# Optimization experiments

Hardware: AMD Instinct MI355X
Metric: run time of the kernel (lower is better)

## Reference

```python
import jax, jax.numpy as jnp
import numpy as np

T = 32          # timesteps
GAIN = 1.0      # input_gain
TAU = 2.0       # LIF membrane time constant
VTH = 1.0       # v_threshold
VRESET = 0.0    # v_reset (hard reset)
ALPHA = 2.0     # ATan surrogate alpha


@jax.custom_vjp
def heaviside_atan(x):
    # forward: Heaviside spike; backward: ATan surrogate gradient
    return (x >= 0).astype(x.dtype)

def _hs_fwd(x):
    return heaviside_atan(x), x

def _hs_bwd(x, g):
    # d/dx ATan surrogate: (alpha/2) / (1 + (pi/2 * alpha * x)^2)
    return (g * (ALPHA / 2.0) / (1.0 + (jnp.pi / 2.0 * ALPHA * x) ** 2),)

heaviside_atan.defvjp(_hs_fwd, _hs_bwd)


def lif_multistep(cur_seq):
    """Multi-step LIF over cur_seq [T, B, H]; hard reset, detach_reset=True."""
    def step(v, x):
        # charge: v = v + (x - (v - v_reset)) / tau
        v = v + (x - (v - VRESET)) / TAU
        spike = heaviside_atan(v - VTH)
        sd = jax.lax.stop_gradient(spike)  # detach_reset
        v = (1.0 - sd) * v + sd * VRESET   # hard reset
        return v, spike

    v0 = jnp.full(cur_seq.shape[1:], VRESET, dtype=cur_seq.dtype)
    _, spikes = jax.lax.scan(step, v0, cur_seq)
    return spikes


def setup_inputs() -> dict:
    key = jax.random.key(0)
    ks = jax.random.split(key, 4)

    def xavier(k, o, i):
        lim = np.sqrt(6.0 / (i + o)).astype(np.float32)
        return jax.random.uniform(k, (o, i), minval=-lim, maxval=lim, dtype=jnp.float32)

    x_flat = jax.random.uniform(ks[0], (512, 784), dtype=jnp.float32)
    W0 = xavier(ks[1], 1024, 784)
    b0 = jnp.zeros((1024,), jnp.float32)
    W1 = xavier(ks[2], 1024, 1024)
    b1 = jnp.zeros((1024,), jnp.float32)
    W2 = xavier(ks[3], 10, 1024)
    b2 = jnp.zeros((10,), jnp.float32)
    return {"x_flat": x_flat, "W0": W0, "b0": b0, "W1": W1, "b1": b1, "W2": W2, "b2": b2}


def reference(x_flat, W0, b0, W1, b1, W2, b2):
    # repeat_static_input: [B, 784] -> [T, B, 784]
    h = jnp.broadcast_to(x_flat * GAIN, (T,) + x_flat.shape)
    count = None
    for W, b in ((W0, b0), (W1, b1), (W2, b2)):
        cur = jnp.einsum('tbi,oi->tbo', h, W) + b  # fc over all timesteps
        spk = lif_multistep(cur)                   # [T, B, out]
        count = spk.sum(axis=0)                    # spike counts [B, out]
        h = spk
    # predict() returns argmax(count); return the final count (logits) here
    return count
```

## Files before the change

kernel.cpp:

```cpp
#include <hip/hip_runtime.h>
#include <hip/hip_bf16.h>
#include <stdint.h>


typedef __bf16 bf16x8 __attribute__((ext_vector_type(8)));
typedef float  f32x4  __attribute__((ext_vector_type(4)));
typedef unsigned short u16x8 __attribute__((ext_vector_type(8)));

__device__ __forceinline__ unsigned short csel(float v, int sel) {
  __hip_bfloat16 h = __float2bfloat16(v);
  if (sel == 0) return __builtin_bit_cast(unsigned short, h);
  float r1 = v - __bfloat162float(h);
  __hip_bfloat16 m = __float2bfloat16(r1);
  if (sel == 1) return __builtin_bit_cast(unsigned short, m);
  float r2 = r1 - __bfloat162float(m);
  __hip_bfloat16 l = __float2bfloat16(r2);
  return __builtin_bit_cast(unsigned short, l);
}

__global__ __launch_bounds__(256, 2) void gemm0t_k(const float* __restrict__ x,
                                                   const float* __restrict__ W0,
                                                   const float* __restrict__ W1,
                                                   float* __restrict__ W1T,
                                                   float* __restrict__ Cpart) {
  __shared__ __align__(16) char smem[16512];
  const int bid = blockIdx.x, tid = threadIdx.x;

  if (bid >= 320) {
    float (*t)[33] = (float(*)[33])smem;
    int tt = bid - 320;
    int c0 = (tt & 31) * 32, r0 = (tt >> 5) * 32;
    int lx = tid & 31, ly = tid >> 5;
#pragma unroll
    for (int i = 0; i < 32; i += 8)
      t[ly + i][lx] = W1[(size_t)(r0 + ly + i) * 1024 + (c0 + lx)];
    __syncthreads();
#pragma unroll
    for (int i = 0; i < 32; i += 8)
      W1T[(size_t)(c0 + ly + i) * 1024 + (r0 + lx)] = t[lx][ly + i];
    return;
  }

  const int bx = bid & 3, by = (bid >> 2) & 7, bz = bid >> 5;
  const int wave = tid >> 6, lane = tid & 63, quad = lane >> 4, l16 = lane & 15;
  const int wm = (wave >> 1) * 64, wn = (wave & 1) * 64;
  const int mbase = bx * 128, nbase = by * 128, kbase = bz * 480;
  const int swz = (l16 >> 1) & 3;

  const int r = tid >> 1, h = tid & 1;
  const int sw = (r >> 1) & 3;
  const int swap = sw & 1;
  char* adst = smem + r * 64 + 32 * (h ^ (sw >> 1));
  char* bdst = smem + 8192 + r * 64 + 32 * (h ^ (sw >> 1));
  const float* xr = x + (size_t)(mbase + r) * 784;
  const float* wr = W0 + (size_t)(nbase + r) * 784;

  f32x4 acc[4][4] = {};

  for (int kk = kbase; kk < kbase + 480; kk += 32) {
    const int s = kk / 800;
    const int k0 = kk - s * 800 + h * 16;
    const int selA = (s == 2 || s == 3) ? 1 : ((s == 5) ? 2 : 0);
    const int selB = (s == 1 || s == 3) ? 1 : ((s == 4) ? 2 : 0);
    {
      float v[16];
#pragma unroll
      for (int q = 0; q < 4; ++q) {
        int kq = k0 + q * 4;
        if (kq < 784) {
          f32x4 t4 = *(const f32x4*)(xr + kq);
          v[q*4+0] = t4[0]; v[q*4+1] = t4[1]; v[q*4+2] = t4[2]; v[q*4+3] = t4[3];
        } else {
          v[q*4+0] = 0.f; v[q*4+1] = 0.f; v[q*4+2] = 0.f; v[q*4+3] = 0.f;
        }
      }
      u16x8 c0v, c1v;
#pragma unroll
      for (int j = 0; j < 8; ++j) c0v[j] = csel(v[j], selA);
#pragma unroll
      for (int j = 0; j < 8; ++j) c1v[j] = csel(v[8 + j], selA);
      *(u16x8*)(adst + (swap ? 16 : 0)) = c0v;
      *(u16x8*)(adst + (swap ? 0 : 16)) = c1v;
    }
    {
      float v[16];
#pragma unroll
      for (int q = 0; q < 4; ++q) {
        int kq = k0 + q * 4;
        if (kq < 784) {
          f32x4 t4 = *(const f32x4*)(wr + kq);
          v[q*4+0] = t4[0]; v[q*4+1] = t4[1]; v[q*4+2] = t4[2]; v[q*4+3] = t4[3];
        } else {
          v[q*4+0] = 0.f; v[q*4+1] = 0.f; v[q*4+2] = 0.f; v[q*4+3] = 0.f;
        }
      }
      u16x8 c0v, c1v;
#pragma unroll
      for (int j = 0; j < 8; ++j) c0v[j] = csel(v[j], selB);
#pragma unroll
      for (int j = 0; j < 8; ++j) c1v[j] = csel(v[8 + j], selB);
      *(u16x8*)(bdst + (swap ? 16 : 0)) = c0v;
      *(u16x8*)(bdst + (swap ? 0 : 16)) = c1v;
    }
    __syncthreads();

    const __bf16* Ab = (const __bf16*)smem;
    const __bf16* Bb = Ab + 128 * 32;
    bf16x8 af[4], bfr[4];
#pragma unroll
    for (int i = 0; i < 4; ++i)
      af[i] = *(const bf16x8*)(Ab + (wm + i * 16 + l16) * 32 + ((quad ^ swz) * 8));
#pragma unroll
    for (int j = 0; j < 4; ++j)
      bfr[j] = *(const bf16x8*)(Bb + (wn + j * 16 + l16) * 32 + ((quad ^ swz) * 8));
#pragma unroll
    for (int i = 0; i < 4; ++i)
#pragma unroll
      for (int j = 0; j < 4; ++j)
        acc[i][j] = __builtin_amdgcn_mfma_f32_16x16x32_bf16(af[i], bfr[j], acc[i][j], 0, 0, 0);
    __syncthreads();
  }

  float* Cz = Cpart + (size_t)bz * 512 * 1024;
#pragma unroll
  for (int i = 0; i < 4; ++i)
#pragma unroll
    for (int j = 0; j < 4; ++j)
#pragma unroll
      for (int rr = 0; rr < 4; ++rr) {
        int m = mbase + wm + i * 16 + quad * 4 + rr;
        int n = nbase + wn + j * 16 + l16;
        Cz[(size_t)m * 1024 + n] = acc[i][j][rr];
      }
}

struct TailSM {
  unsigned short sidx[1024];
  int sseg[33];
  int mtot;
  unsigned l2i[1024];
  unsigned l2w[1024];
  union {
    struct { int whist[16][33]; int clstot[33]; int clsofs[34]; int wofs[16][33]; } s3;
    struct { int wtot[16]; int wbase[16]; } s4;
    struct { float sW2[10 * 1025]; float scur[320]; } s5;
  } u;
};

__global__ __launch_bounds__(1024) void tail_k(const float* __restrict__ Cpart,
                                               const float* __restrict__ b0,
                                               const float* __restrict__ W1T,
                                               const float* __restrict__ b1,
                                               const float* __restrict__ W2,
                                               const float* __restrict__ b2,
                                               float* __restrict__ out) {
  __shared__ TailSM sm;
  const int b = blockIdx.x, o = threadIdx.x;
  const int wave = o >> 6, lane = o & 63;

  {
    float cur = 0.f;
#pragma unroll
    for (int z = 0; z < 10; ++z)
      cur += Cpart[(size_t)z * 512 * 1024 + (size_t)b * 1024 + o];
    cur += b0[o];
    float v = 0.f;
    unsigned word = 0u;
#pragma unroll
    for (int t = 0; t < 32; ++t) {
      v = v + (cur - v) * 0.5f;
      if (v >= 1.0f) { word |= 1u << t; v = 0.f; }
    }
    int n = word ? (__builtin_ctz(word) + 1) : 0;
    unsigned long long mymask = 0ull;
#pragma unroll 1
    for (int c = 1; c <= 32; ++c) {
      unsigned long long m = __ballot(n == c);
      if (lane == 0) sm.u.s3.whist[wave][c] = __popcll(m);
      if (n == c) mymask = m;
    }
    __syncthreads();
    if (o < 32) {
      int c = o + 1, s = 0;
#pragma unroll
      for (int w = 0; w < 16; ++w) s += sm.u.s3.whist[w][c];
      sm.u.s3.clstot[c] = s;
    }
    __syncthreads();
    if (o == 0) {
      int run = 0;
#pragma unroll
      for (int c = 1; c <= 32; ++c) { sm.u.s3.clsofs[c] = run; run += sm.u.s3.clstot[c]; }
      sm.u.s3.clsofs[33] = run;
    }
    __syncthreads();
    if (o < 32) {
      int c = o + 1, s = sm.u.s3.clsofs[c];
#pragma unroll
      for (int w = 0; w < 16; ++w) { sm.u.s3.wofs[w][c] = s; s += sm.u.s3.whist[w][c]; }
    }
    __syncthreads();
    if (n) {
      int pos = sm.u.s3.wofs[wave][n] + __popcll(mymask & ((1ull << lane) - 1ull));
      sm.sidx[pos] = (unsigned short)o;
    }
    if (o < 33) sm.sseg[o] = sm.u.s3.clsofs[o + 1];
  }
  __syncthreads();

  {
    float S[32];
#pragma unroll
    for (int c = 0; c < 32; ++c) {
      int j0 = __builtin_amdgcn_readfirstlane((c == 0) ? 0 : sm.sseg[c - 1]);
      int j1 = __builtin_amdgcn_readfirstlane(sm.sseg[c]);
      float s = 0.f;
      for (int j = j0; j < j1; ++j)
        s += W1T[(size_t)sm.sidx[j] * 1024 + o];
      S[c] = s;
    }
    const float bias = b1[o];
    float v = 0.f;
    unsigned word = 0u;
#pragma unroll
    for (int t = 0; t < 32; ++t) {
      float cur = 0.f;
#pragma unroll
      for (int c = 1; c <= 32; ++c)
        if ((t + 1) % c == 0) cur += S[c - 1];
      float xc = cur + bias;
      v = v + (xc - v) * 0.5f;
      if (v >= 1.0f) { word |= 1u << t; v = 0.f; }
    }
    bool act = (word != 0u);
    unsigned long long m = __ballot(act);
    if (lane == 0) sm.u.s4.wtot[wave] = __popcll(m);
    __syncthreads();
    if (o == 0) {
      int s = 0;
#pragma unroll
      for (int i = 0; i < 16; ++i) { sm.u.s4.wbase[i] = s; s += sm.u.s4.wtot[i]; }
      sm.mtot = s;
    }
    __syncthreads();
    if (act) {
      int pos = sm.u.s4.wbase[wave] + __popcll(m & ((1ull << lane) - 1ull));
      sm.l2i[pos] = (unsigned)o;
      sm.l2w[pos] = word;
    }
  }
  __syncthreads();

  {
    for (int i = o; i < 10240; i += 1024)
      sm.u.s5.sW2[(i >> 10) * 1025 + (i & 1023)] = W2[i];
    __syncthreads();
    const int mtot = sm.mtot;
    if (o < 320) {
      int t = o / 10, c = o - t * 10;
      float acc = 0.f;
      for (int j = 0; j < mtot; ++j) {
        unsigned wd = sm.l2w[j];
        float wv = sm.u.s5.sW2[c * 1025 + sm.l2i[j]];
        acc += ((wd >> t) & 1u) ? wv : 0.f;
      }
      sm.u.s5.scur[o] = acc;
    }
    __syncthreads();
    if (o < 10) {
      float v = 0.f, cnt2 = 0.f, bias = b2[o];
#pragma unroll
      for (int tt = 0; tt < 32; ++tt) {
        float xc = sm.u.s5.scur[tt * 10 + o] + bias;
        v = v + (xc - v) * 0.5f;
        if (v >= 1.0f) { cnt2 += 1.f; v = 0.f; }
      }
      out[(size_t)b * 10 + o] = cnt2;
    }
  }
}

extern "C" void kernel_launch(void* const* d_in, const int* in_sizes, int n_in,
                              void* d_out, int out_size, void* d_ws, size_t ws_size,
                              hipStream_t stream) {
  const float* x  = (const float*)d_in[0];
  const float* W0 = (const float*)d_in[1];
  const float* b0 = (const float*)d_in[2];
  const float* W1 = (const float*)d_in[3];
  const float* b1 = (const float*)d_in[4];
  const float* W2 = (const float*)d_in[5];
  const float* b2 = (const float*)d_in[6];
  float* out = (float*)d_out;

  char* ws = (char*)d_ws;
  size_t off = 0;
  auto alloc = [&](size_t bytes) -> char* {
    char* p = ws + off;
    off += (bytes + 255) & ~(size_t)255;
    return p;
  };
  float* Cpart = (float*)alloc((size_t)10 * 512 * 1024 * 4);
  float* W1T   = (float*)alloc((size_t)1024 * 1024 * 4);
  (void)ws_size;

  gemm0t_k<<<1344, 256, 0, stream>>>(x, W0, W1, W1T, Cpart);
  tail_k<<<512, 1024, 0, stream>>>(Cpart, b0, W1T, b1, W2, b2, out);
}
```

Measured before the change: 125.0 us.

## Pre-split fp32 operands into bf16 triplets and stream them via direct global-to-LDS loads

Adds a prep kernel that splits x and W0 once into hi/mid/lo bf16 parts, laid out as six concatenated K-segments. The GEMM can then load bf16 tiles straight into shared memory with global_load_lds, with no per-tile splitting inside the loop. Before, each block recomputed the split for every K tile. The change costs an extra kernel launch and about 15MB of extra global traffic to write and re-read the bf16 buffers.

```diff
diff --git a/kernel.cpp b/kernel.cpp
--- a/kernel.cpp
+++ b/kernel.cpp
@@ -5,30 +5,52 @@
 
 typedef __bf16 bf16x8 __attribute__((ext_vector_type(8)));
 typedef float  f32x4  __attribute__((ext_vector_type(4)));
-typedef unsigned short u16x8 __attribute__((ext_vector_type(8)));
-
-__device__ __forceinline__ unsigned short csel(float v, int sel) {
-  __hip_bfloat16 h = __float2bfloat16(v);
-  if (sel == 0) return __builtin_bit_cast(unsigned short, h);
+
+__device__ __forceinline__ void gload16(const void* g, void* l) {
+  __builtin_amdgcn_global_load_lds((const __attribute__((address_space(1))) void*)g,
+                                   (__attribute__((address_space(3))) void*)l,
+                                   16, 0, 0);
+}
+
+__device__ __forceinline__ void bsplit3(float v, __hip_bfloat16& h,
+                                        __hip_bfloat16& m, __hip_bfloat16& l) {
+  h = __float2bfloat16(v);
   float r1 = v - __bfloat162float(h);
-  __hip_bfloat16 m = __float2bfloat16(r1);
-  if (sel == 1) return __builtin_bit_cast(unsigned short, m);
+  m = __float2bfloat16(r1);
   float r2 = r1 - __bfloat162float(m);
-  __hip_bfloat16 l = __float2bfloat16(r2);
-  return __builtin_bit_cast(unsigned short, l);
-}
-
-__global__ __launch_bounds__(256, 2) void gemm0t_k(const float* __restrict__ x,
-                                                   const float* __restrict__ W0,
-                                                   const float* __restrict__ W1,
-                                                   float* __restrict__ W1T,
-                                                   float* __restrict__ Cpart) {
-  __shared__ __align__(16) char smem[16512];
+  l = __float2bfloat16(r2);
+}
+
+__global__ __launch_bounds__(256) void prep_k(const float* __restrict__ x,
+                                              const float* __restrict__ W0,
+                                              const float* __restrict__ W1,
+                                              __hip_bfloat16* __restrict__ Ax,
+                                              __hip_bfloat16* __restrict__ Bw,
+                                              float* __restrict__ W1T) {
   const int bid = blockIdx.x, tid = threadIdx.x;
-
-  if (bid >= 320) {
-    float (*t)[33] = (float(*)[33])smem;
-    int tt = bid - 320;
+  if (bid < 1600) {
+    int i = bid * 256 + tid;
+    int m = i / 800, k = i - m * 800;
+    float v = (k < 784) ? x[(size_t)m * 784 + k] : 0.f;
+    __hip_bfloat16 h, mm, l;
+    bsplit3(v, h, mm, l);
+    size_t base = (size_t)m * 4800;
+    Ax[base + k] = h;         Ax[base + 800 + k] = h;
+    Ax[base + 1600 + k] = mm; Ax[base + 2400 + k] = mm;
+    Ax[base + 3200 + k] = h;  Ax[base + 4000 + k] = l;
+  } else if (bid < 4800) {
+    int i = (bid - 1600) * 256 + tid;
+    int n = i / 800, k = i - n * 800;
+    float v = (k < 784) ? W0[(size_t)n * 784 + k] : 0.f;
+    __hip_bfloat16 h, mm, l;
+    bsplit3(v, h, mm, l);
+    size_t base = (size_t)n * 4800;
+    Bw[base + k] = h;         Bw[base + 800 + k] = mm;
+    Bw[base + 1600 + k] = h;  Bw[base + 2400 + k] = mm;
+    Bw[base + 3200 + k] = l;  Bw[base + 4000 + k] = h;
+  } else {
+    __shared__ float t[32][33];
+    int tt = bid - 4800;
     int c0 = (tt & 31) * 32, r0 = (tt >> 5) * 32;
     int lx = tid & 31, ly = tid >> 5;
 #pragma unroll
@@ -38,74 +60,35 @@
 #pragma unroll
     for (int i = 0; i < 32; i += 8)
       W1T[(size_t)(c0 + ly + i) * 1024 + (r0 + lx)] = t[lx][ly + i];
-    return;
-  }
-
-  const int bx = bid & 3, by = (bid >> 2) & 7, bz = bid >> 5;
+  }
+}
+
+__global__ __launch_bounds__(256, 2) void gemm0_k(const __hip_bfloat16* __restrict__ A,
+                                                  const __hip_bfloat16* __restrict__ B,
+                                                  float* __restrict__ Cpart) {
+  __shared__ __align__(16) __hip_bfloat16 As[128 * 32];
+  __shared__ __align__(16) __hip_bfloat16 Bs[128 * 32];
+  const int tid = threadIdx.x;
   const int wave = tid >> 6, lane = tid & 63, quad = lane >> 4, l16 = lane & 15;
   const int wm = (wave >> 1) * 64, wn = (wave & 1) * 64;
-  const int mbase = bx * 128, nbase = by * 128, kbase = bz * 480;
+  const int mbase = blockIdx.x * 128, nbase = blockIdx.y * 128;
+  const int kbase = blockIdx.z * 480;
+  const int srow = lane >> 2;
+  const int gq = (lane & 3) ^ ((lane >> 3) & 3);
   const int swz = (l16 >> 1) & 3;
-
-  const int r = tid >> 1, h = tid & 1;
-  const int sw = (r >> 1) & 3;
-  const int swap = sw & 1;
-  char* adst = smem + r * 64 + 32 * (h ^ (sw >> 1));
-  char* bdst = smem + 8192 + r * 64 + 32 * (h ^ (sw >> 1));
-  const float* xr = x + (size_t)(mbase + r) * 784;
-  const float* wr = W0 + (size_t)(nbase + r) * 784;
-
   f32x4 acc[4][4] = {};
-
   for (int kk = kbase; kk < kbase + 480; kk += 32) {
-    const int s = kk / 800;
-    const int k0 = kk - s * 800 + h * 16;
-    const int selA = (s == 2 || s == 3) ? 1 : ((s == 5) ? 2 : 0);
-    const int selB = (s == 1 || s == 3) ? 1 : ((s == 4) ? 2 : 0);
-    {
-      float v[16];
-#pragma unroll
-      for (int q = 0; q < 4; ++q) {
-        int kq = k0 + q * 4;
-        if (kq < 784) {
-          f32x4 t4 = *(const f32x4*)(xr + kq);
-          v[q*4+0] = t4[0]; v[q*4+1] = t4[1]; v[q*4+2] = t4[2]; v[q*4+3] = t4[3];
-        } else {
-          v[q*4+0] = 0.f; v[q*4+1] = 0.f; v[q*4+2] = 0.f; v[q*4+3] = 0.f;
-        }
-      }
-      u16x8 c0v, c1v;
-#pragma unroll
-      for (int j = 0; j < 8; ++j) c0v[j] = csel(v[j], selA);
-#pragma unroll
-      for (int j = 0; j < 8; ++j) c1v[j] = csel(v[8 + j], selA);
-      *(u16x8*)(adst + (swap ? 16 : 0)) = c0v;
-      *(u16x8*)(adst + (swap ? 0 : 16)) = c1v;
-    }
-    {
-      float v[16];
-#pragma unroll
-      for (int q = 0; q < 4; ++q) {
-        int kq = k0 + q * 4;
-        if (kq < 784) {
-          f32x4 t4 = *(const f32x4*)(wr + kq);
-          v[q*4+0] = t4[0]; v[q*4+1] = t4[1]; v[q*4+2] = t4[2]; v[q*4+3] = t4[3];
-        } else {
-          v[q*4+0] = 0.f; v[q*4+1] = 0.f; v[q*4+2] = 0.f; v[q*4+3] = 0.f;
-        }
-      }
-      u16x8 c0v, c1v;
-#pragma unroll
-      for (int j = 0; j < 8; ++j) c0v[j] = csel(v[j], selB);
-#pragma unroll
-      for (int j = 0; j < 8; ++j) c1v[j] = csel(v[8 + j], selB);
-      *(u16x8*)(bdst + (swap ? 16 : 0)) = c0v;
-      *(u16x8*)(bdst + (swap ? 0 : 16)) = c1v;
-    }
-    __syncthreads();
-
-    const __bf16* Ab = (const __bf16*)smem;
-    const __bf16* Bb = Ab + 128 * 32;
+#pragma unroll
+    for (int r = 0; r < 2; ++r) {
+      int grp = wave * 2 + r;
+      gload16(A + (size_t)(mbase + grp * 16 + srow) * 4800 + kk + gq * 8,
+              (char*)As + grp * 1024);
+      gload16(B + (size_t)(nbase + grp * 16 + srow) * 4800 + kk + gq * 8,
+              (char*)Bs + grp * 1024);
+    }
+    __syncthreads();
+    const __bf16* Ab = (const __bf16*)As;
+    const __bf16* Bb = (const __bf16*)Bs;
     bf16x8 af[4], bfr[4];
 #pragma unroll
     for (int i = 0; i < 4; ++i)
@@ -120,17 +103,16 @@
         acc[i][j] = __builtin_amdgcn_mfma_f32_16x16x32_bf16(af[i], bfr[j], acc[i][j], 0, 0, 0);
     __syncthreads();
   }
-
-  float* Cz = Cpart + (size_t)bz * 512 * 1024;
+  float* Cz = Cpart + (size_t)blockIdx.z * 512 * 1024;
 #pragma unroll
   for (int i = 0; i < 4; ++i)
 #pragma unroll
     for (int j = 0; j < 4; ++j)
 #pragma unroll
-      for (int rr = 0; rr < 4; ++rr) {
-        int m = mbase + wm + i * 16 + quad * 4 + rr;
+      for (int r = 0; r < 4; ++r) {
+        int m = mbase + wm + i * 16 + quad * 4 + r;
         int n = nbase + wn + j * 16 + l16;
-        Cz[(size_t)m * 1024 + n] = acc[i][j][rr];
+        Cz[(size_t)m * 1024 + n] = acc[i][j][r];
       }
 }
 
@@ -299,10 +281,13 @@
     off += (bytes + 255) & ~(size_t)255;
     return p;
   };
-  float* Cpart = (float*)alloc((size_t)10 * 512 * 1024 * 4);
-  float* W1T   = (float*)alloc((size_t)1024 * 1024 * 4);
+  __hip_bfloat16* Ax    = (__hip_bfloat16*)alloc((size_t)512 * 4800 * 2);
+  __hip_bfloat16* Bw    = (__hip_bfloat16*)alloc((size_t)1024 * 4800 * 2);
+  float*          Cpart = (float*)alloc((size_t)10 * 512 * 1024 * 4);
+  float*          W1T   = (float*)alloc((size_t)1024 * 1024 * 4);
   (void)ws_size;
 
-  gemm0t_k<<<1344, 256, 0, stream>>>(x, W0, W1, W1T, Cpart);
+  prep_k<<<5824, 256, 0, stream>>>(x, W0, W1, Ax, Bw, W1T);
+  gemm0_k<<<dim3(4, 8, 10), 256, 0, stream>>>(Ax, Bw, Cpart);
   tail_k<<<512, 1024, 0, stream>>>(Cpart, b0, W1T, b1, W2, b2, out);
 }
```

After: 114.2 us. 1.09x faster.
